# Optimization experiments

Hardware: AMD Instinct MI355X
Metric: run time of the kernel (lower is better)

Reference implementation:

```python
import jax, jax.numpy as jnp
import numpy as np

B, T, D_IN, HID, NB, NCLS = 256, 512, 64, 64, 10, 2


def ferro_basis(x, centers, widths, coeffs):
    """KAN-style ferroelectric basis expansion.
    x: (N, in_dim); centers/widths: (num_basis,); coeffs: (in_dim, num_basis, out_dim)
    returns (N, out_dim).
    """
    phi = jnp.tanh((x[..., None] - centers) / widths)  # (N, in_dim, num_basis)
    return jnp.einsum('bik,iko->bo', phi, coeffs)


def setup_inputs() -> dict:
    key = jax.random.key(0)
    ks = jax.random.split(key, 8)
    sc = 1.0 / np.sqrt(D_IN * NB)
    inp = {
        'x': jax.random.normal(ks[0], (B, T, D_IN), dtype=jnp.float32),
        'lift_centers': jnp.linspace(-1.0, 1.0, NB, dtype=jnp.float32),
        'lift_widths': jnp.full((NB,), 0.5, dtype=jnp.float32),
        'lift_coeffs': jax.random.normal(ks[1], (D_IN, NB, HID), dtype=jnp.float32) * sc,
        'rnn_centers': jnp.linspace(-1.0, 1.0, NB, dtype=jnp.float32),
        'rnn_widths': jnp.full((NB,), 0.5, dtype=jnp.float32),
        'rnn_coeffs': jax.random.normal(ks[2], (HID, NB, HID), dtype=jnp.float32) * (1.0 / np.sqrt(HID * NB)),
        'head_centers': jnp.linspace(-1.0, 1.0, NB, dtype=jnp.float32),
        'head_widths': jnp.full((NB,), 0.5, dtype=jnp.float32),
        'head_coeffs': jax.random.normal(ks[3], (HID, NB, HID), dtype=jnp.float32) * (1.0 / np.sqrt(HID * NB)),
        'head_W': jax.random.normal(ks[4], (HID, NCLS), dtype=jnp.float32) * (1.0 / np.sqrt(HID)),
        'head_b': jnp.zeros((NCLS,), dtype=jnp.float32),
    }
    return inp


def reference(x, lift_centers, lift_widths, lift_coeffs,
              rnn_centers, rnn_widths, rnn_coeffs,
              head_centers, head_widths, head_coeffs,
              head_W, head_b):
    b, t, d = x.shape
    # NODE_Encoder: t = linspace(0, T, steps=1) -> single time point, so odeint
    # returns h0 unchanged; z_t == lift(x_t). Lift applied to every timestep
    # (as in the original per-t loop), vectorized over B*T.
    z = ferro_basis(x.reshape(b * t, d), lift_centers, lift_widths, lift_coeffs)
    z = z.reshape(b, t, -1)  # (B, T, HID)
    # FullyNonlinearKANCell: combined[:, :hidden] == x_phi, so h_t = sigmoid(input_basis(z_t));
    # the recurrence is degenerate and the final h depends only on the last timestep.
    h = jax.nn.sigmoid(ferro_basis(z[:, -1, :], rnn_centers, rnn_widths, rnn_coeffs))
    # dropout: eval mode -> identity
    phi = jax.nn.sigmoid(ferro_basis(h, head_centers, head_widths, head_coeffs))
    logits = phi @ head_W + head_b  # (B, num_classes)
    return logits
```

## Files before the change

kernel.cpp:

```cpp
#include <hip/hip_runtime.h>
#include <math.h>

#define BB    256
#define TT    512
#define DIN   64
#define HIDD  64
#define NBAS  10
#define NCLS  2

#define NTHR  256
#define NW    4
#define EPW   160
#define NF4   40

__device__ __forceinline__ float sigmoidf_(float v) {
    return 1.0f / (1.0f + expf(-v));
}

__global__ __launch_bounds__(NTHR, 1) void kan_fwd(
    const float* __restrict__ x,
    const float* __restrict__ lift_c, const float* __restrict__ lift_w, const float* __restrict__ lift_coef,
    const float* __restrict__ rnn_c,  const float* __restrict__ rnn_w,  const float* __restrict__ rnn_coef,
    const float* __restrict__ head_c, const float* __restrict__ head_w, const float* __restrict__ head_coef,
    const float* __restrict__ W, const float* __restrict__ bvec,
    float* __restrict__ out)
{
    const int b    = blockIdx.x;
    const int t    = threadIdx.x;
    const int l    = t & 63;
    const int w    = t >> 6;
    const int esub = l >> 4;
    const int og   = (l & 15) << 2;

    __shared__ float act[DIN];
    __shared__ __align__(16) float part[NW][DIN];

    const int i0 = (w << 4) + l / NBAS,          k0 = l % NBAS;
    const int i1 = (w << 4) + (64 + l) / NBAS,   k1 = (64 + l) % NBAS;
    const int i2 = (w << 4) + (128 + l) / NBAS,  k2 = (128 + l) % NBAS;

    const float* xb = x + ((size_t)b * TT + (TT - 1)) * DIN;
    const float x0 = xb[i0];
    const float x1 = xb[i1];
    const float x2 = (l < 32) ? xb[i2] : 0.0f;

    const float lc0 = lift_c[k0], lw0 = 1.0f / lift_w[k0];
    const float lc1 = lift_c[k1], lw1 = 1.0f / lift_w[k1];
    const float lc2 = lift_c[k2], lw2 = 1.0f / lift_w[k2];
    const float rc0 = rnn_c[k0],  rw0 = 1.0f / rnn_w[k0];
    const float rc1 = rnn_c[k1],  rw1 = 1.0f / rnn_w[k1];
    const float rc2 = rnn_c[k2],  rw2 = 1.0f / rnn_w[k2];
    const float hc0 = head_c[k0], hw0 = 1.0f / head_w[k0];
    const float hc1 = head_c[k1], hw1 = 1.0f / head_w[k1];
    const float hc2 = head_c[k2], hw2 = 1.0f / head_w[k2];
    float W0 = 0.0f, W1 = 0.0f;
    if (t < DIN) { W0 = W[t * NCLS + 0]; W1 = W[t * NCLS + 1]; }

    const size_t fbase = (size_t)(EPW * w + esub) * 16 + (og >> 2);
    const float4* fA = (const float4*)lift_coef + fbase;
    const float4* fB = (const float4*)rnn_coef  + fbase;
    const float4* fC = (const float4*)head_coef + fbase;

    #define CONTRACT(ACC, PV0, PV1, PV2, CARR)                                  \
        {                                                                       \
            _Pragma("unroll")                                                   \
            for (int j = 0; j < NF4; ++j) {                                     \
                float pj;                                                       \
                if (j < 16)      pj = __shfl((PV0), esub + 4 * j);              \
                else if (j < 32) pj = __shfl((PV1), esub + 4 * j - 64);         \
                else             pj = __shfl((PV2), esub + 4 * j - 128);        \
                const float4 cf = (CARR)[j];                                    \
                (ACC).x = fmaf(pj, cf.x, (ACC).x);                              \
                (ACC).y = fmaf(pj, cf.y, (ACC).y);                              \
                (ACC).z = fmaf(pj, cf.z, (ACC).z);                              \
                (ACC).w = fmaf(pj, cf.w, (ACC).w);                              \
            }                                                                   \
        }

    #define XREDUCE(ACC)                                                        \
        {                                                                       \
            _Pragma("unroll")                                                   \
            for (int off = 16; off < 64; off <<= 1) {                           \
                (ACC).x += __shfl_xor((ACC).x, off);                            \
                (ACC).y += __shfl_xor((ACC).y, off);                            \
                (ACC).z += __shfl_xor((ACC).z, off);                            \
                (ACC).w += __shfl_xor((ACC).w, off);                            \
            }                                                                   \
        }

    float4 c1[NF4];
    #pragma unroll
    for (int j = 0; j < NF4; ++j) c1[j] = fA[j * 64];

    float pv0 = tanhf((x0 - lc0) * lw0);
    float pv1 = tanhf((x1 - lc1) * lw1);
    float pv2 = (l < 32) ? tanhf((x2 - lc2) * lw2) : 0.0f;

    float4 a = make_float4(0.f, 0.f, 0.f, 0.f);
    CONTRACT(a, pv0, pv1, pv2, c1);

    float4 c2[NF4];
    #pragma unroll
    for (int j = 0; j < NF4; ++j) c2[j] = fB[j * 64];

    XREDUCE(a);
    if (esub == 0) *(float4*)&part[w][og] = a;
    __syncthreads();
    if (t < DIN)
        act[t] = part[0][t] + part[1][t] + part[2][t] + part[3][t];
    __syncthreads();

    pv0 = tanhf((act[i0] - rc0) * rw0);
    pv1 = tanhf((act[i1] - rc1) * rw1);
    pv2 = (l < 32) ? tanhf((act[i2] - rc2) * rw2) : 0.0f;

    a = make_float4(0.f, 0.f, 0.f, 0.f);
    CONTRACT(a, pv0, pv1, pv2, c2);

    float4 c3[NF4];
    #pragma unroll
    for (int j = 0; j < NF4; ++j) c3[j] = fC[j * 64];

    XREDUCE(a);
    if (esub == 0) *(float4*)&part[w][og] = a;
    __syncthreads();
    if (t < DIN)
        act[t] = sigmoidf_(part[0][t] + part[1][t] + part[2][t] + part[3][t]);
    __syncthreads();

    pv0 = tanhf((act[i0] - hc0) * hw0);
    pv1 = tanhf((act[i1] - hc1) * hw1);
    pv2 = (l < 32) ? tanhf((act[i2] - hc2) * hw2) : 0.0f;

    a = make_float4(0.f, 0.f, 0.f, 0.f);
    CONTRACT(a, pv0, pv1, pv2, c3);
    XREDUCE(a);
    if (esub == 0) *(float4*)&part[w][og] = a;
    __syncthreads();

    if (t < DIN) {
        float s = part[0][t] + part[1][t] + part[2][t] + part[3][t];
        s = sigmoidf_(s);
        float p0 = s * W0;
        float p1 = s * W1;
        #pragma unroll
        for (int off = 32; off > 0; off >>= 1) {
            p0 += __shfl_down(p0, off);
            p1 += __shfl_down(p1, off);
        }
        if (t == 0) {
            out[b * NCLS + 0] = p0 + bvec[0];
            out[b * NCLS + 1] = p1 + bvec[1];
        }
    }

    #undef CONTRACT
    #undef XREDUCE
}

extern "C" void kernel_launch(void* const* d_in, const int* in_sizes, int n_in,
                              void* d_out, int out_size, void* d_ws, size_t ws_size,
                              hipStream_t stream) {
    const float* x          = (const float*)d_in[0];
    const float* lift_c     = (const float*)d_in[1];
    const float* lift_w     = (const float*)d_in[2];
    const float* lift_coef  = (const float*)d_in[3];
    const float* rnn_c      = (const float*)d_in[4];
    const float* rnn_w      = (const float*)d_in[5];
    const float* rnn_coef   = (const float*)d_in[6];
    const float* head_c     = (const float*)d_in[7];
    const float* head_w     = (const float*)d_in[8];
    const float* head_coef  = (const float*)d_in[9];
    const float* W          = (const float*)d_in[10];
    const float* bvec       = (const float*)d_in[11];
    float* out              = (float*)d_out;

    kan_fwd<<<dim3(BB), dim3(NTHR), 0, stream>>>(
        x, lift_c, lift_w, lift_coef,
        rnn_c, rnn_w, rnn_coef,
        head_c, head_w, head_coef,
        W, bvec, out);
}
```

Measured before the change: 13.69 us.

## Split KAN contraction across eight waves and prefetch two coefficient sets

Doubles the block to 512 threads (8 waves), so each wave covers 8 input features (80 basis elements, 20 float4 rows) instead of 16. The index mapping, shuffles and cross-wave reduction are rewritten to match. The rnn coefficients are now loaded up front together with the lift coefficients, which gives more memory-level parallelism on this latency-bound kernel. In exchange there are more partial sums to reduce, heavier barriers with 8 waves, and the launch bound now targets 2 blocks per CU.

Measured after the change: 13.58 us. About the same (-0.8%).

```diff
diff --git a/kernel.cpp b/kernel.cpp
--- a/kernel.cpp
+++ b/kernel.cpp
@@ -8,16 +8,16 @@
 #define NBAS  10
 #define NCLS  2
 
-#define NTHR  256
-#define NW    4
-#define EPW   160
-#define NF4   40
+#define NTHR  512
+#define NW    8
+#define EPW   80
+#define NF4   20
 
 __device__ __forceinline__ float sigmoidf_(float v) {
     return 1.0f / (1.0f + expf(-v));
 }
 
-__global__ __launch_bounds__(NTHR, 1) void kan_fwd(
+__global__ __launch_bounds__(NTHR, 2) void kan_fwd(
     const float* __restrict__ x,
     const float* __restrict__ lift_c, const float* __restrict__ lift_w, const float* __restrict__ lift_coef,
     const float* __restrict__ rnn_c,  const float* __restrict__ rnn_w,  const float* __restrict__ rnn_coef,
@@ -35,24 +35,20 @@
     __shared__ float act[DIN];
     __shared__ __align__(16) float part[NW][DIN];
 
-    const int i0 = (w << 4) + l / NBAS,          k0 = l % NBAS;
-    const int i1 = (w << 4) + (64 + l) / NBAS,   k1 = (64 + l) % NBAS;
-    const int i2 = (w << 4) + (128 + l) / NBAS,  k2 = (128 + l) % NBAS;
+    const int i0 = (w << 3) + l / NBAS,        k0 = l % NBAS;
+    const int i1 = (w << 3) + (64 + l) / NBAS, k1 = (64 + l) % NBAS;
+    const bool ph1 = (l < (EPW - 64));
 
     const float* xb = x + ((size_t)b * TT + (TT - 1)) * DIN;
     const float x0 = xb[i0];
-    const float x1 = xb[i1];
-    const float x2 = (l < 32) ? xb[i2] : 0.0f;
+    const float x1 = ph1 ? xb[i1] : 0.0f;
 
     const float lc0 = lift_c[k0], lw0 = 1.0f / lift_w[k0];
     const float lc1 = lift_c[k1], lw1 = 1.0f / lift_w[k1];
-    const float lc2 = lift_c[k2], lw2 = 1.0f / lift_w[k2];
     const float rc0 = rnn_c[k0],  rw0 = 1.0f / rnn_w[k0];
     const float rc1 = rnn_c[k1],  rw1 = 1.0f / rnn_w[k1];
-    const float rc2 = rnn_c[k2],  rw2 = 1.0f / rnn_w[k2];
     const float hc0 = head_c[k0], hw0 = 1.0f / head_w[k0];
     const float hc1 = head_c[k1], hw1 = 1.0f / head_w[k1];
-    const float hc2 = head_c[k2], hw2 = 1.0f / head_w[k2];
     float W0 = 0.0f, W1 = 0.0f;
     if (t < DIN) { W0 = W[t * NCLS + 0]; W1 = W[t * NCLS + 1]; }
 
@@ -61,14 +57,12 @@
     const float4* fB = (const float4*)rnn_coef  + fbase;
     const float4* fC = (const float4*)head_coef + fbase;
 
-    #define CONTRACT(ACC, PV0, PV1, PV2, CARR)                                  \
+    #define CONTRACT(ACC, PV0, PV1, CARR)                                       \
         {                                                                       \
             _Pragma("unroll")                                                   \
             for (int j = 0; j < NF4; ++j) {                                     \
-                float pj;                                                       \
-                if (j < 16)      pj = __shfl((PV0), esub + 4 * j);              \
-                else if (j < 32) pj = __shfl((PV1), esub + 4 * j - 64);         \
-                else             pj = __shfl((PV2), esub + 4 * j - 128);        \
+                const float pj = (j < 16) ? __shfl((PV0), esub + 4 * j)         \
+                                          : __shfl((PV1), esub + 4 * (j - 16)); \
                 const float4 cf = (CARR)[j];                                    \
                 (ACC).x = fmaf(pj, cf.x, (ACC).x);                              \
                 (ACC).y = fmaf(pj, cf.y, (ACC).y);                              \
@@ -88,34 +82,17 @@
             }                                                                   \
         }
 
-    float4 c1[NF4];
+    float4 c1[NF4], c2[NF4];
     #pragma unroll
     for (int j = 0; j < NF4; ++j) c1[j] = fA[j * 64];
-
-    float pv0 = tanhf((x0 - lc0) * lw0);
-    float pv1 = tanhf((x1 - lc1) * lw1);
-    float pv2 = (l < 32) ? tanhf((x2 - lc2) * lw2) : 0.0f;
-
-    float4 a = make_float4(0.f, 0.f, 0.f, 0.f);
-    CONTRACT(a, pv0, pv1, pv2, c1);
-
-    float4 c2[NF4];
     #pragma unroll
     for (int j = 0; j < NF4; ++j) c2[j] = fB[j * 64];
 
-    XREDUCE(a);
-    if (esub == 0) *(float4*)&part[w][og] = a;
-    __syncthreads();
-    if (t < DIN)
-        act[t] = part[0][t] + part[1][t] + part[2][t] + part[3][t];
-    __syncthreads();
+    float pv0 = tanhf((x0 - lc0) * lw0);
+    float pv1 = ph1 ? tanhf((x1 - lc1) * lw1) : 0.0f;
 
-    pv0 = tanhf((act[i0] - rc0) * rw0);
-    pv1 = tanhf((act[i1] - rc1) * rw1);
-    pv2 = (l < 32) ? tanhf((act[i2] - rc2) * rw2) : 0.0f;
-
-    a = make_float4(0.f, 0.f, 0.f, 0.f);
-    CONTRACT(a, pv0, pv1, pv2, c2);
+    float4 a = make_float4(0.f, 0.f, 0.f, 0.f);
+    CONTRACT(a, pv0, pv1, c1);
 
     float4 c3[NF4];
     #pragma unroll
@@ -124,22 +101,43 @@
     XREDUCE(a);
     if (esub == 0) *(float4*)&part[w][og] = a;
     __syncthreads();
-    if (t < DIN)
-        act[t] = sigmoidf_(part[0][t] + part[1][t] + part[2][t] + part[3][t]);
+    if (t < DIN) {
+        float s = 0.0f;
+        #pragma unroll
+        for (int ww = 0; ww < NW; ++ww) s += part[ww][t];
+        act[t] = s;
+    }
+    __syncthreads();
+
+    pv0 = tanhf((act[i0] - rc0) * rw0);
+    pv1 = ph1 ? tanhf((act[i1] - rc1) * rw1) : 0.0f;
+
+    a = make_float4(0.f, 0.f, 0.f, 0.f);
+    CONTRACT(a, pv0, pv1, c2);
+    XREDUCE(a);
+    if (esub == 0) *(float4*)&part[w][og] = a;
+    __syncthreads();
+    if (t < DIN) {
+        float s = 0.0f;
+        #pragma unroll
+        for (int ww = 0; ww < NW; ++ww) s += part[ww][t];
+        act[t] = sigmoidf_(s);
+    }
     __syncthreads();
 
     pv0 = tanhf((act[i0] - hc0) * hw0);
-    pv1 = tanhf((act[i1] - hc1) * hw1);
-    pv2 = (l < 32) ? tanhf((act[i2] - hc2) * hw2) : 0.0f;
+    pv1 = ph1 ? tanhf((act[i1] - hc1) * hw1) : 0.0f;
 
     a = make_float4(0.f, 0.f, 0.f, 0.f);
-    CONTRACT(a, pv0, pv1, pv2, c3);
+    CONTRACT(a, pv0, pv1, c3);
     XREDUCE(a);
     if (esub == 0) *(float4*)&part[w][og] = a;
     __syncthreads();
 
     if (t < DIN) {
-        float s = part[0][t] + part[1][t] + part[2][t] + part[3][t];
+        float s = 0.0f;
+        #pragma unroll
+        for (int ww = 0; ww < NW; ++ww) s += part[ww][t];
         s = sigmoidf_(s);
         float p0 = s * W0;
         float p1 = s * W1;
```
